# Kernel optimization log

Hardware: AMD Instinct MI355X
Metric: run time of the kernel (lower is better)

## Reference

```python
import jax, jax.numpy as jnp
import numpy as np

N, D_IN, D_K = 8192, 512, 64


def setup_inputs() -> dict:
    key = jax.random.key(0)
    k0, k1, k2, k3 = jax.random.split(key, 4)
    return {
        "inputs": jax.random.normal(k0, (N, D_IN), dtype=jnp.float32),
        "Wq": jax.random.normal(k1, (D_K, D_IN), dtype=jnp.float32),
        "Wk": jax.random.normal(k2, (D_K, D_IN), dtype=jnp.float32),
        "Wv": jax.random.normal(k3, (D_K, D_IN), dtype=jnp.float32),
    }


def reference(inputs, Wq, Wk, Wv):
    # nn.Linear(bias=False): x @ W.T, W has shape [out, in]
    q = inputs @ Wq.T  # [N, Dk]
    k = inputs @ Wk.T  # [N, Dk]
    v = inputs @ Wv.T  # [N, Dk]
    scaled = (q @ k.T) / jnp.sqrt(jnp.float32(D_K))  # [N, N]
    attn = jax.nn.softmax(scaled, axis=1)            # softmax over keys (dim=1)
    # weighted = values[:,None] * attn.T[:,:,None]; sum over dim 0 == attn @ v
    return attn @ v  # [N, Dk]
```

## Files before the change

kernel.cpp:

```cpp
#include <hip/hip_runtime.h>
#include <hip/hip_bf16.h>


#define N_TOK 8192
#define D_INN 512
#define DK    64
#define QSCALE 0.18033688011112042f

typedef __attribute__((ext_vector_type(8))) short bf16x8;
typedef __attribute__((ext_vector_type(4))) float f32x4;

#define GLOAD_LDS16(gsrc, ldst) \
  __builtin_amdgcn_global_load_lds( \
      (const __attribute__((address_space(1))) unsigned int*)(gsrc), \
      (__attribute__((address_space(3))) unsigned int*)(ldst), 16, 0, 0)

static __device__ __forceinline__ unsigned f2bf_u(float f) {
  union { float f; unsigned u; } v; v.f = f;
  return (v.u + 0x7FFFu + ((v.u >> 16) & 1u)) >> 16;
}
static __device__ __forceinline__ unsigned short f2bf(float f) { return (unsigned short)f2bf_u(f); }
static __device__ __forceinline__ float bf2f(unsigned short h) {
  union { unsigned u; float f; } v; v.u = ((unsigned)h) << 16; return v.f;
}
static __device__ __forceinline__ unsigned truncpk(float a, float b) {
  union { float f; unsigned u; } x, y; x.f = a; y.f = b;
  return (x.u >> 16) | (y.u & 0xFFFF0000u);
}
static __device__ __forceinline__ void split2(float a, float b, unsigned& hi, unsigned& lo) {
  unsigned ha = f2bf_u(a), hb = f2bf_u(b);
  float ra = a - bf2f((unsigned short)ha);
  float rb = b - bf2f((unsigned short)hb);
  hi = ha | (hb << 16);
  lo = f2bf_u(ra) | (f2bf_u(rb) << 16);
}
static __device__ __forceinline__ void split8(const float* p, bf16x8& hi, bf16x8& lo) {
  float4 a = *(const float4*)p;
  float4 b = *(const float4*)(p + 4);
  union { unsigned u[4]; bf16x8 v; } H, L;
  split2(a.x, a.y, H.u[0], L.u[0]);
  split2(a.z, a.w, H.u[1], L.u[1]);
  split2(b.x, b.y, H.u[2], L.u[2]);
  split2(b.z, b.w, H.u[3], L.u[3]);
  hi = H.v; lo = L.v;
}
static __device__ __forceinline__ bf16x8 round8(const float* p) {
  float4 a = *(const float4*)p;
  float4 b = *(const float4*)(p + 4);
  union { unsigned u[4]; bf16x8 v; } H;
  H.u[0] = f2bf_u(a.x) | (f2bf_u(a.y) << 16);
  H.u[1] = f2bf_u(a.z) | (f2bf_u(a.w) << 16);
  H.u[2] = f2bf_u(b.x) | (f2bf_u(b.y) << 16);
  H.u[3] = f2bf_u(b.z) | (f2bf_u(b.w) << 16);
  return H.v;
}

__global__ __launch_bounds__(256, 2) void qkv3(
    const float* __restrict__ X,
    const float* __restrict__ Wq, const float* __restrict__ Wk, const float* __restrict__ Wv,
    unsigned short* __restrict__ qhp, unsigned short* __restrict__ qlp,
    unsigned short* __restrict__ kph, unsigned short* __restrict__ kpl,
    unsigned short* __restrict__ vp) {
  const int tid = threadIdx.x, w = tid >> 6, l = tid & 63;
  const int l15 = l & 15, g = l >> 4;
  const int t0 = blockIdx.x * 16;
  const int dq = w * 16;

  f32x4 aq = {0.f, 0.f, 0.f, 0.f}, ak = aq, av = aq;

  for (int kc = 0; kc < D_INN; kc += 32) {
    bf16x8 ah, al;
    split8(X + (t0 + l15) * D_INN + kc + g * 8, ah, al);

    const int woff = (dq + l15) * D_INN + kc + g * 8;
    bf16x8 bqh, bql, bkh, bkl;
    split8(Wq + woff, bqh, bql);
    split8(Wk + woff, bkh, bkl);
    bf16x8 bvh = round8(Wv + woff);

    aq = __builtin_amdgcn_mfma_f32_16x16x32_bf16(ah, bqh, aq, 0, 0, 0);
    aq = __builtin_amdgcn_mfma_f32_16x16x32_bf16(ah, bql, aq, 0, 0, 0);
    aq = __builtin_amdgcn_mfma_f32_16x16x32_bf16(al, bqh, aq, 0, 0, 0);
    ak = __builtin_amdgcn_mfma_f32_16x16x32_bf16(ah, bkh, ak, 0, 0, 0);
    ak = __builtin_amdgcn_mfma_f32_16x16x32_bf16(ah, bkl, ak, 0, 0, 0);
    ak = __builtin_amdgcn_mfma_f32_16x16x32_bf16(al, bkh, ak, 0, 0, 0);
    av = __builtin_amdgcn_mfma_f32_16x16x32_bf16(ah, bvh, av, 0, 0, 0);
    av = __builtin_amdgcn_mfma_f32_16x16x32_bf16(al, bvh, av, 0, 0, 0);
  }

#pragma unroll
  for (int r = 0; r < 4; r++) {
    float v = aq[r] * QSCALE;
    int row = t0 + g * 4 + r;
    unsigned short h = f2bf(v);
    qhp[row * DK + dq + l15] = h;
    qlp[row * DK + dq + l15] = f2bf(v - bf2f(h));
  }
#pragma unroll
  for (int r = 0; r < 4; r++) {
    float v = ak[r];
    int t = t0 + g * 4 + r;
    int d = dq + l15;
    int off = (t >> 5) * 2048 + ((t >> 4) & 1) * 1024 + (d >> 5) * 512 +
              ((t & 15) + (((d >> 3) & 3) << 4)) * 8 + (d & 7);
    unsigned short h = f2bf(v);
    kph[off] = h;
    kpl[off] = f2bf(v - bf2f(h));
  }
  {
    int tg = t0 + g * 4;
    int d = dq + l15;
    int off = (tg >> 5) * 2048 + (d >> 4) * 512 +
              (((d & 15) + (((tg >> 3) & 3) << 4))) * 8 + (tg & 7);
    uint2 pk;
    pk.x = f2bf_u(av[0]) | (f2bf_u(av[1]) << 16);
    pk.y = f2bf_u(av[2]) | (f2bf_u(av[3]) << 16);
    *(uint2*)(vp + off) = pk;
  }
}

static __device__ __forceinline__ void stage_tile(
    const unsigned short* __restrict__ kph, const unsigned short* __restrict__ kpl,
    const unsigned short* __restrict__ vp, int kti,
    unsigned short* lds, int w, int l) {
  const unsigned short* kb = kph + kti * 2048;
  const unsigned short* lb = kpl + kti * 2048;
  const unsigned short* vb = vp + kti * 2048;
#pragma unroll
  for (int j = 0; j < 6; ++j) {
    int chunk = w * 6 + j;
    const unsigned short* src = (chunk < 8) ? kb : ((chunk < 16) ? lb : vb);
    GLOAD_LDS16(src + (chunk & 7) * 512 + l * 8, lds + chunk * 512);
  }
}

__global__ __launch_bounds__(256, 2) void attn6(
    const unsigned short* __restrict__ qhp, const unsigned short* __restrict__ qlp,
    const unsigned short* __restrict__ kph, const unsigned short* __restrict__ kpl,
    const unsigned short* __restrict__ vp,
    unsigned short* __restrict__ pnb, float* __restrict__ pden, float* __restrict__ pM) {
  __shared__ unsigned short kv_lds[2 * 12288];
  __shared__ unsigned short P_lds[4 * 16 * 72];

  const int tid = threadIdx.x, w = tid >> 6, l = tid & 63;
  const int l15 = l & 15, g = l >> 4;
  const int qblk = blockIdx.x >> 3, ks = blockIdx.x & 7;
  const int wq0 = qblk * 128 + w * 32;

  bf16x8 qhf[2][2], qlf[2][2];
#pragma unroll
  for (int u = 0; u < 2; u++)
#pragma unroll
    for (int c = 0; c < 2; c++) {
      int row = wq0 + u * 16 + l15;
      qhf[u][c] = *(const bf16x8*)(qhp + row * DK + c * 32 + g * 8);
      qlf[u][c] = *(const bf16x8*)(qlp + row * DK + c * 32 + g * 8);
    }

  const short onec = (short)0x3F80;
  const bf16x8 ones = {onec, onec, onec, onec, onec, onec, onec, onec};

  f32x4 accO[2][4], accL[2];
  float m[2] = {-1e30f, -1e30f};
#pragma unroll
  for (int u = 0; u < 2; u++) {
    accL[u] = f32x4{0.f, 0.f, 0.f, 0.f};
#pragma unroll
    for (int ds = 0; ds < 4; ds++) accO[u][ds] = f32x4{0.f, 0.f, 0.f, 0.f};
  }

  const int kti0 = ks * 32;
  stage_tile(kph, kpl, vp, kti0, kv_lds, w, l);
  __syncthreads();

  for (int t = 0; t < 16; ++t) {
    const int cb = (t & 1) ? 12288 : 0;
    const int pb = 12288 - cb;
    const int ktin = (t < 15) ? (kti0 + 2 * t + 2) : (kti0 + 2 * t);
    stage_tile(kph, kpl, vp, ktin, kv_lds + pb, w, l);

    const unsigned short* Kh = kv_lds + cb;
    const unsigned short* Kl = Kh + 4096;
    const unsigned short* Vv = Kh + 8192;

    f32x4 st[2][4];
#pragma unroll
    for (int s = 0; s < 4; s++) {
      bf16x8 khf[2], klf[2];
#pragma unroll
      for (int c = 0; c < 2; c++) {
        const int off = (s >> 1) * 2048 + (s & 1) * 1024 + c * 512 + l * 8;
        khf[c] = *(const bf16x8*)(Kh + off);
        klf[c] = *(const bf16x8*)(Kl + off);
      }
      __builtin_amdgcn_s_setprio(1);
#pragma unroll
      for (int u = 0; u < 2; u++) {
        f32x4 sa = {0.f, 0.f, 0.f, 0.f};
        sa = __builtin_amdgcn_mfma_f32_16x16x32_bf16(khf[0], qhf[u][0], sa, 0, 0, 0);
        sa = __builtin_amdgcn_mfma_f32_16x16x32_bf16(khf[1], qhf[u][1], sa, 0, 0, 0);
        sa = __builtin_amdgcn_mfma_f32_16x16x32_bf16(khf[0], qlf[u][0], sa, 0, 0, 0);
        sa = __builtin_amdgcn_mfma_f32_16x16x32_bf16(khf[1], qlf[u][1], sa, 0, 0, 0);
        sa = __builtin_amdgcn_mfma_f32_16x16x32_bf16(klf[0], qhf[u][0], sa, 0, 0, 0);
        sa = __builtin_amdgcn_mfma_f32_16x16x32_bf16(klf[1], qhf[u][1], sa, 0, 0, 0);
        st[u][s] = sa;
      }
      __builtin_amdgcn_s_setprio(0);
    }

    bf16x8 vb[4][2];
#pragma unroll
    for (int ds = 0; ds < 4; ds++)
#pragma unroll
      for (int c = 0; c < 2; c++)
        vb[ds][c] = *(const bf16x8*)(Vv + c * 2048 + ds * 512 + l * 8);

#pragma unroll
    for (int u = 0; u < 2; u++) {
      float t0m = fmaxf(fmaxf(st[u][0][0], st[u][0][1]), fmaxf(st[u][0][2], st[u][0][3]));
      float t1m = fmaxf(fmaxf(st[u][1][0], st[u][1][1]), fmaxf(st[u][1][2], st[u][1][3]));
      float t2m = fmaxf(fmaxf(st[u][2][0], st[u][2][1]), fmaxf(st[u][2][2], st[u][2][3]));
      float t3m = fmaxf(fmaxf(st[u][3][0], st[u][3][1]), fmaxf(st[u][3][2], st[u][3][3]));
      float tm = fmaxf(fmaxf(t0m, t1m), fmaxf(t2m, t3m));
      tm = fmaxf(tm, __shfl_xor(tm, 16, 64));
      tm = fmaxf(tm, __shfl_xor(tm, 32, 64));
      if (__any(tm > m[u] + 11.0f)) {
        float mn = fmaxf(m[u], tm);
        float fac = exp2f(m[u] - mn);
        m[u] = mn;
#pragma unroll
        for (int r = 0; r < 4; r++) {
          float fr = __shfl(fac, g * 4 + r, 64);
          accL[u][r] *= fr;
#pragma unroll
          for (int ds = 0; ds < 4; ds++) accO[u][ds][r] *= fr;
        }
      }
      const int base = (w * 16 + l15) * 72;
#pragma unroll
      for (int s = 0; s < 4; s++) {
        float p0 = exp2f(st[u][s][0] - m[u]);
        float p1 = exp2f(st[u][s][1] - m[u]);
        float p2 = exp2f(st[u][s][2] - m[u]);
        float p3 = exp2f(st[u][s][3] - m[u]);
        *(unsigned*)&P_lds[base + s * 16 + g * 4]     = truncpk(p0, p1);
        *(unsigned*)&P_lds[base + s * 16 + g * 4 + 2] = truncpk(p2, p3);
      }
      bf16x8 pa0 = *(const bf16x8*)&P_lds[base + g * 8];
      bf16x8 pa1 = *(const bf16x8*)&P_lds[base + 32 + g * 8];
      __builtin_amdgcn_s_setprio(1);
      accL[u] = __builtin_amdgcn_mfma_f32_16x16x32_bf16(pa0, ones, accL[u], 0, 0, 0);
      accL[u] = __builtin_amdgcn_mfma_f32_16x16x32_bf16(pa1, ones, accL[u], 0, 0, 0);
#pragma unroll
      for (int ds = 0; ds < 4; ds++) {
        accO[u][ds] = __builtin_amdgcn_mfma_f32_16x16x32_bf16(pa0, vb[ds][0], accO[u][ds], 0, 0, 0);
        accO[u][ds] = __builtin_amdgcn_mfma_f32_16x16x32_bf16(pa1, vb[ds][1], accO[u][ds], 0, 0, 0);
      }
      __builtin_amdgcn_s_setprio(0);
    }

    __syncthreads();
  }

#pragma unroll
  for (int u = 0; u < 2; u++) {
#pragma unroll
    for (int ds = 0; ds < 4; ds++)
#pragma unroll
      for (int r = 0; r < 4; r++)
        pnb[(size_t)ks * (N_TOK * DK) + (wq0 + u * 16 + g * 4 + r) * DK + ds * 16 + l15] =
            f2bf(accO[u][ds][r]);
    if (l15 == 0) {
#pragma unroll
      for (int r = 0; r < 4; r++) pden[ks * N_TOK + wq0 + u * 16 + g * 4 + r] = accL[u][r];
    }
    if (g == 0) pM[ks * N_TOK + wq0 + u * 16 + l15] = m[u];
  }
}

__global__ __launch_bounds__(256) void merge8(
    const unsigned short* __restrict__ pnb, const float* __restrict__ pden,
    const float* __restrict__ pM, float* __restrict__ out) {
  int i = blockIdx.x * 256 + threadIdx.x;
  int q = i >> 6, d = i & 63;
  float M = -1e30f;
#pragma unroll
  for (int s = 0; s < 8; s++) M = fmaxf(M, pM[s * N_TOK + q]);
  float num = 0.f, den = 0.f;
#pragma unroll
  for (int s = 0; s < 8; s++) {
    float e = exp2f(pM[s * N_TOK + q] - M);
    num += bf2f(pnb[(size_t)s * (N_TOK * DK) + q * DK + d]) * e;
    den += pden[s * N_TOK + q] * e;
  }
  out[i] = num / den;
}

extern "C" void kernel_launch(void* const* d_in, const int* in_sizes, int n_in,
                              void* d_out, int out_size, void* d_ws, size_t ws_size,
                              hipStream_t stream) {
  (void)in_sizes; (void)n_in; (void)out_size; (void)ws_size;
  const float* X  = (const float*)d_in[0];
  const float* Wq = (const float*)d_in[1];
  const float* Wk = (const float*)d_in[2];
  const float* Wv = (const float*)d_in[3];

  char* base = (char*)d_ws;
  unsigned short* pnb = (unsigned short*)(base);
  unsigned short* qhp = (unsigned short*)(base + 16777216);
  unsigned short* qlp = (unsigned short*)(base + 17825792);
  unsigned short* kph = (unsigned short*)(base + 18874368);
  unsigned short* kpl = (unsigned short*)(base + 19922944);
  unsigned short* vp  = (unsigned short*)(base + 20971520);
  float* pden = (float*)(base + 22020096);
  float* pM   = (float*)(base + 22544384);

  qkv3<<<N_TOK / 16, 256, 0, stream>>>(X, Wq, Wk, Wv, qhp, qlp, kph, kpl, vp);
  attn6<<<512, 256, 0, stream>>>(qhp, qlp, kph, kpl, vp, pnb, pden, pM);
  merge8<<<(N_TOK * DK) / 256, 256, 0, stream>>>(pnb, pden, pM, (float*)d_out);
}
```

Measured before the change: 151.6 us.

## Restructure attention to 8 waves of 16 query rows with 32-key tiles

The attention kernel moves from 4 waves each handling 32 query rows over 64-key tiles to 8 waves each handling 16 rows over 32-key tiles, with 512 threads per block and a smaller double-buffered LDS footprint. Per-wave register state (accumulators, Q fragments) is halved, which is meant to raise occupancy and hide latency, but the loop now has twice as many iterations and barriers. The exp2-based softmax with the log2e-folded Q scale is replaced by __expf with a plain 1/8 scale, and the rescale threshold drops from 11 to 8.

Measured after the change: 147.9 us. -2.4%, faster.

```diff
diff --git a/kernel.cpp b/kernel.cpp
--- a/kernel.cpp
+++ b/kernel.cpp
@@ -5,7 +5,6 @@
 #define N_TOK 8192
 #define D_INN 512
 #define DK    64
-#define QSCALE 0.18033688011112042f
 
 typedef __attribute__((ext_vector_type(8))) short bf16x8;
 typedef __attribute__((ext_vector_type(4))) float f32x4;
@@ -90,7 +89,7 @@
 
 #pragma unroll
   for (int r = 0; r < 4; r++) {
-    float v = aq[r] * QSCALE;
+    float v = aq[r] * 0.125f;
     int row = t0 + g * 4 + r;
     unsigned short h = f2bf(v);
     qhp[row * DK + dq + l15] = h;
@@ -119,163 +118,141 @@
   }
 }
 
-static __device__ __forceinline__ void stage_tile(
+static __device__ __forceinline__ void stage_tile32(
     const unsigned short* __restrict__ kph, const unsigned short* __restrict__ kpl,
     const unsigned short* __restrict__ vp, int kti,
     unsigned short* lds, int w, int l) {
   const unsigned short* kb = kph + kti * 2048;
   const unsigned short* lb = kpl + kti * 2048;
   const unsigned short* vb = vp + kti * 2048;
-#pragma unroll
-  for (int j = 0; j < 6; ++j) {
-    int chunk = w * 6 + j;
-    const unsigned short* src = (chunk < 8) ? kb : ((chunk < 16) ? lb : vb);
-    GLOAD_LDS16(src + (chunk & 7) * 512 + l * 8, lds + chunk * 512);
-  }
-}
-
-__global__ __launch_bounds__(256, 2) void attn6(
+  {
+    int chunk = w;
+    const unsigned short* src = (chunk < 4) ? kb : lb;
+    GLOAD_LDS16(src + (chunk & 3) * 512 + l * 8, lds + chunk * 512);
+  }
+  if (w < 4) {
+    int chunk = 8 + w;
+    GLOAD_LDS16(vb + (chunk & 3) * 512 + l * 8, lds + chunk * 512);
+  }
+}
+
+__global__ __launch_bounds__(512, 4) void attn8(
     const unsigned short* __restrict__ qhp, const unsigned short* __restrict__ qlp,
     const unsigned short* __restrict__ kph, const unsigned short* __restrict__ kpl,
     const unsigned short* __restrict__ vp,
     unsigned short* __restrict__ pnb, float* __restrict__ pden, float* __restrict__ pM) {
-  __shared__ unsigned short kv_lds[2 * 12288];
-  __shared__ unsigned short P_lds[4 * 16 * 72];
+  __shared__ unsigned short kv_lds[2 * 6144];
+  __shared__ unsigned short P_lds[8 * 16 * 40];
 
   const int tid = threadIdx.x, w = tid >> 6, l = tid & 63;
   const int l15 = l & 15, g = l >> 4;
   const int qblk = blockIdx.x >> 3, ks = blockIdx.x & 7;
-  const int wq0 = qblk * 128 + w * 32;
-
-  bf16x8 qhf[2][2], qlf[2][2];
-#pragma unroll
-  for (int u = 0; u < 2; u++)
-#pragma unroll
-    for (int c = 0; c < 2; c++) {
-      int row = wq0 + u * 16 + l15;
-      qhf[u][c] = *(const bf16x8*)(qhp + row * DK + c * 32 + g * 8);
-      qlf[u][c] = *(const bf16x8*)(qlp + row * DK + c * 32 + g * 8);
-    }
+  const int wq0 = qblk * 128 + w * 16;
+
+  bf16x8 qhf[2], qlf[2];
+#pragma unroll
+  for (int c = 0; c < 2; c++) {
+    int row = wq0 + l15;
+    qhf[c] = *(const bf16x8*)(qhp + row * DK + c * 32 + g * 8);
+    qlf[c] = *(const bf16x8*)(qlp + row * DK + c * 32 + g * 8);
+  }
 
   const short onec = (short)0x3F80;
   const bf16x8 ones = {onec, onec, onec, onec, onec, onec, onec, onec};
 
-  f32x4 accO[2][4], accL[2];
-  float m[2] = {-1e30f, -1e30f};
-#pragma unroll
-  for (int u = 0; u < 2; u++) {
-    accL[u] = f32x4{0.f, 0.f, 0.f, 0.f};
-#pragma unroll
-    for (int ds = 0; ds < 4; ds++) accO[u][ds] = f32x4{0.f, 0.f, 0.f, 0.f};
-  }
+  f32x4 accO[4], accL = {0.f, 0.f, 0.f, 0.f};
+  float m = -1e30f;
+#pragma unroll
+  for (int ds = 0; ds < 4; ds++) accO[ds] = f32x4{0.f, 0.f, 0.f, 0.f};
 
   const int kti0 = ks * 32;
-  stage_tile(kph, kpl, vp, kti0, kv_lds, w, l);
+  stage_tile32(kph, kpl, vp, kti0, kv_lds, w, l);
   __syncthreads();
 
-  for (int t = 0; t < 16; ++t) {
-    const int cb = (t & 1) ? 12288 : 0;
-    const int pb = 12288 - cb;
-    const int ktin = (t < 15) ? (kti0 + 2 * t + 2) : (kti0 + 2 * t);
-    stage_tile(kph, kpl, vp, ktin, kv_lds + pb, w, l);
+  for (int t = 0; t < 32; ++t) {
+    const int cb = (t & 1) ? 6144 : 0;
+    const int pb = 6144 - cb;
+    const int ktin = kti0 + ((t < 31) ? (t + 1) : t);
+    stage_tile32(kph, kpl, vp, ktin, kv_lds + pb, w, l);
 
     const unsigned short* Kh = kv_lds + cb;
-    const unsigned short* Kl = Kh + 4096;
-    const unsigned short* Vv = Kh + 8192;
-
-    f32x4 st[2][4];
-#pragma unroll
-    for (int s = 0; s < 4; s++) {
+    const unsigned short* Kl = Kh + 2048;
+    const unsigned short* Vv = Kh + 4096;
+
+    f32x4 st[2];
+#pragma unroll
+    for (int s = 0; s < 2; s++) {
       bf16x8 khf[2], klf[2];
 #pragma unroll
       for (int c = 0; c < 2; c++) {
-        const int off = (s >> 1) * 2048 + (s & 1) * 1024 + c * 512 + l * 8;
+        const int off = s * 1024 + c * 512 + l * 8;
         khf[c] = *(const bf16x8*)(Kh + off);
         klf[c] = *(const bf16x8*)(Kl + off);
       }
       __builtin_amdgcn_s_setprio(1);
-#pragma unroll
-      for (int u = 0; u < 2; u++) {
-        f32x4 sa = {0.f, 0.f, 0.f, 0.f};
-        sa = __builtin_amdgcn_mfma_f32_16x16x32_bf16(khf[0], qhf[u][0], sa, 0, 0, 0);
-        sa = __builtin_amdgcn_mfma_f32_16x16x32_bf16(khf[1], qhf[u][1], sa, 0, 0, 0);
-        sa = __builtin_amdgcn_mfma_f32_16x16x32_bf16(khf[0], qlf[u][0], sa, 0, 0, 0);
-        sa = __builtin_amdgcn_mfma_f32_16x16x32_bf16(khf[1], qlf[u][1], sa, 0, 0, 0);
-        sa = __builtin_amdgcn_mfma_f32_16x16x32_bf16(klf[0], qhf[u][0], sa, 0, 0, 0);
-        sa = __builtin_amdgcn_mfma_f32_16x16x32_bf16(klf[1], qhf[u][1], sa, 0, 0, 0);
-        st[u][s] = sa;
+      f32x4 sa = {0.f, 0.f, 0.f, 0.f};
+      sa = __builtin_amdgcn_mfma_f32_16x16x32_bf16(khf[0], qhf[0], sa, 0, 0, 0);
+      sa = __builtin_amdgcn_mfma_f32_16x16x32_bf16(khf[1], qhf[1], sa, 0, 0, 0);
+      sa = __builtin_amdgcn_mfma_f32_16x16x32_bf16(khf[0], qlf[0], sa, 0, 0, 0);
+      sa = __builtin_amdgcn_mfma_f32_16x16x32_bf16(khf[1], qlf[1], sa, 0, 0, 0);
+      sa = __builtin_amdgcn_mfma_f32_16x16x32_bf16(klf[0], qhf[0], sa, 0, 0, 0);
+      sa = __builtin_amdgcn_mfma_f32_16x16x32_bf16(klf[1], qhf[1], sa, 0, 0, 0);
+      st[s] = sa;
+      __builtin_amdgcn_s_setprio(0);
+    }
+
+    float t0m = fmaxf(fmaxf(st[0][0], st[0][1]), fmaxf(st[0][2], st[0][3]));
+    float t1m = fmaxf(fmaxf(st[1][0], st[1][1]), fmaxf(st[1][2], st[1][3]));
+    float tm = fmaxf(t0m, t1m);
+    tm = fmaxf(tm, __shfl_xor(tm, 16, 64));
+    tm = fmaxf(tm, __shfl_xor(tm, 32, 64));
+    if (__any(tm > m + 8.f)) {
+      float mn = fmaxf(m, tm);
+      float fac = __expf(m - mn);
+      m = mn;
+#pragma unroll
+      for (int r = 0; r < 4; r++) {
+        float fr = __shfl(fac, g * 4 + r, 64);
+        accL[r] *= fr;
+#pragma unroll
+        for (int ds = 0; ds < 4; ds++) accO[ds][r] *= fr;
       }
-      __builtin_amdgcn_s_setprio(0);
-    }
-
-    bf16x8 vb[4][2];
-#pragma unroll
-    for (int ds = 0; ds < 4; ds++)
-#pragma unroll
-      for (int c = 0; c < 2; c++)
-        vb[ds][c] = *(const bf16x8*)(Vv + c * 2048 + ds * 512 + l * 8);
-
-#pragma unroll
-    for (int u = 0; u < 2; u++) {
-      float t0m = fmaxf(fmaxf(st[u][0][0], st[u][0][1]), fmaxf(st[u][0][2], st[u][0][3]));
-      float t1m = fmaxf(fmaxf(st[u][1][0], st[u][1][1]), fmaxf(st[u][1][2], st[u][1][3]));
-      float t2m = fmaxf(fmaxf(st[u][2][0], st[u][2][1]), fmaxf(st[u][2][2], st[u][2][3]));
-      float t3m = fmaxf(fmaxf(st[u][3][0], st[u][3][1]), fmaxf(st[u][3][2], st[u][3][3]));
-      float tm = fmaxf(fmaxf(t0m, t1m), fmaxf(t2m, t3m));
-      tm = fmaxf(tm, __shfl_xor(tm, 16, 64));
-      tm = fmaxf(tm, __shfl_xor(tm, 32, 64));
-      if (__any(tm > m[u] + 11.0f)) {
-        float mn = fmaxf(m[u], tm);
-        float fac = exp2f(m[u] - mn);
-        m[u] = mn;
-#pragma unroll
-        for (int r = 0; r < 4; r++) {
-          float fr = __shfl(fac, g * 4 + r, 64);
-          accL[u][r] *= fr;
-#pragma unroll
-          for (int ds = 0; ds < 4; ds++) accO[u][ds][r] *= fr;
-        }
-      }
-      const int base = (w * 16 + l15) * 72;
-#pragma unroll
-      for (int s = 0; s < 4; s++) {
-        float p0 = exp2f(st[u][s][0] - m[u]);
-        float p1 = exp2f(st[u][s][1] - m[u]);
-        float p2 = exp2f(st[u][s][2] - m[u]);
-        float p3 = exp2f(st[u][s][3] - m[u]);
-        *(unsigned*)&P_lds[base + s * 16 + g * 4]     = truncpk(p0, p1);
-        *(unsigned*)&P_lds[base + s * 16 + g * 4 + 2] = truncpk(p2, p3);
-      }
-      bf16x8 pa0 = *(const bf16x8*)&P_lds[base + g * 8];
-      bf16x8 pa1 = *(const bf16x8*)&P_lds[base + 32 + g * 8];
-      __builtin_amdgcn_s_setprio(1);
-      accL[u] = __builtin_amdgcn_mfma_f32_16x16x32_bf16(pa0, ones, accL[u], 0, 0, 0);
-      accL[u] = __builtin_amdgcn_mfma_f32_16x16x32_bf16(pa1, ones, accL[u], 0, 0, 0);
-#pragma unroll
-      for (int ds = 0; ds < 4; ds++) {
-        accO[u][ds] = __builtin_amdgcn_mfma_f32_16x16x32_bf16(pa0, vb[ds][0], accO[u][ds], 0, 0, 0);
-        accO[u][ds] = __builtin_amdgcn_mfma_f32_16x16x32_bf16(pa1, vb[ds][1], accO[u][ds], 0, 0, 0);
-      }
-      __builtin_amdgcn_s_setprio(0);
-    }
+    }
+    const int base = (w * 16 + l15) * 40;
+#pragma unroll
+    for (int s = 0; s < 2; s++) {
+      float p0 = __expf(st[s][0] - m);
+      float p1 = __expf(st[s][1] - m);
+      float p2 = __expf(st[s][2] - m);
+      float p3 = __expf(st[s][3] - m);
+      *(unsigned*)&P_lds[base + s * 16 + g * 4]     = truncpk(p0, p1);
+      *(unsigned*)&P_lds[base + s * 16 + g * 4 + 2] = truncpk(p2, p3);
+    }
+    bf16x8 pa = *(const bf16x8*)&P_lds[base + g * 8];
+
+    __builtin_amdgcn_s_setprio(1);
+    accL = __builtin_amdgcn_mfma_f32_16x16x32_bf16(pa, ones, accL, 0, 0, 0);
+#pragma unroll
+    for (int ds = 0; ds < 4; ds++) {
+      bf16x8 vb = *(const bf16x8*)(Vv + ds * 512 + l * 8);
+      accO[ds] = __builtin_amdgcn_mfma_f32_16x16x32_bf16(pa, vb, accO[ds], 0, 0, 0);
+    }
+    __builtin_amdgcn_s_setprio(0);
 
     __syncthreads();
   }
 
 #pragma unroll
-  for (int u = 0; u < 2; u++) {
-#pragma unroll
-    for (int ds = 0; ds < 4; ds++)
-#pragma unroll
-      for (int r = 0; r < 4; r++)
-        pnb[(size_t)ks * (N_TOK * DK) + (wq0 + u * 16 + g * 4 + r) * DK + ds * 16 + l15] =
-            f2bf(accO[u][ds][r]);
-    if (l15 == 0) {
-#pragma unroll
-      for (int r = 0; r < 4; r++) pden[ks * N_TOK + wq0 + u * 16 + g * 4 + r] = accL[u][r];
-    }
-    if (g == 0) pM[ks * N_TOK + wq0 + u * 16 + l15] = m[u];
-  }
+  for (int ds = 0; ds < 4; ds++)
+#pragma unroll
+    for (int r = 0; r < 4; r++)
+      pnb[(size_t)ks * (N_TOK * DK) + (wq0 + g * 4 + r) * DK + ds * 16 + l15] =
+          f2bf(accO[ds][r]);
+  if (l15 == 0) {
+#pragma unroll
+    for (int r = 0; r < 4; r++) pden[ks * N_TOK + wq0 + g * 4 + r] = accL[r];
+  }
+  if (g == 0) pM[ks * N_TOK + wq0 + l15] = m;
 }
 
 __global__ __launch_bounds__(256) void merge8(
@@ -289,7 +266,7 @@
   float num = 0.f, den = 0.f;
 #pragma unroll
   for (int s = 0; s < 8; s++) {
-    float e = exp2f(pM[s * N_TOK + q] - M);
+    float e = __expf(pM[s * N_TOK + q] - M);
     num += bf2f(pnb[(size_t)s * (N_TOK * DK) + q * DK + d]) * e;
     den += pden[s * N_TOK + q] * e;
   }
@@ -316,6 +293,6 @@
   float* pM   = (float*)(base + 22544384);
 
   qkv3<<<N_TOK / 16, 256, 0, stream>>>(X, Wq, Wk, Wv, qhp, qlp, kph, kpl, vp);
-  attn6<<<512, 256, 0, stream>>>(qhp, qlp, kph, kpl, vp, pnb, pden, pM);
+  attn8<<<512, 512, 0, stream>>>(qhp, qlp, kph, kpl, vp, pnb, pden, pM);
   merge8<<<(N_TOK * DK) / 256, 256, 0, stream>>>(pnb, pden, pM, (float*)d_out);
 }
```
